# Kernel optimization log

Hardware: AMD Instinct MI355X
Metric: run time of the kernel (lower is better)

Reference implementation:

```python
import jax, jax.numpy as jnp
import numpy as np

B = 2048      # batch
C = 200       # n_country
F = 32        # n_feat_country == n_input
H = 256       # n_hidden


def setup_inputs() -> dict:
    key = jax.random.key(0)
    ks = jax.random.split(key, 9)
    x = jax.random.normal(ks[0], (B, C * F), dtype=jnp.float32)
    transition = jax.random.uniform(ks[1], (C, C), dtype=jnp.float32) / C
    W1 = jax.random.normal(ks[2], (F, H), dtype=jnp.float32) * (1.0 / np.sqrt(F))
    b1 = jax.random.normal(ks[3], (H,), dtype=jnp.float32) * 0.01
    W2 = jax.random.normal(ks[4], (H, H), dtype=jnp.float32) * (1.0 / np.sqrt(H))
    b2 = jax.random.normal(ks[5], (H,), dtype=jnp.float32) * 0.01
    W3 = jax.random.normal(ks[6], (H, 1), dtype=jnp.float32) * (1.0 / np.sqrt(H))
    b3 = jax.random.normal(ks[7], (1,), dtype=jnp.float32) * 0.01
    return {"x": x, "transition": transition, "W1": W1, "b1": b1,
            "W2": W2, "b2": b2, "W3": W3, "b3": b3}


def reference(x, transition, W1, b1, W2, b2, W3, b3):
    Bsz, N = x.shape
    Cn = transition.shape[0]
    Ff = N // Cn
    xc = x.reshape(Bsz, Cn, Ff)            # per-country feature blocks
    S = xc[..., 0]                          # [B, C] susceptible (feature 0)
    I = xc[..., 1]                          # [B, C] infected   (feature 1)
    # transition-weighted neighbor aggregation (the python loop == one GEMM)
    sinflow = S @ transition                # [B, C]
    iinflow = I @ transition                # [B, C]
    outflow = 1.0 - jnp.diag(transition)    # [C]
    # shared tiny MLP applied per country (vectorized over C)
    h = jax.nn.relu(jnp.einsum('bcf,fh->bch', xc, W1) + b1)
    h = jax.nn.relu(jnp.einsum('bch,hk->bck', h, W2) + b2)
    lamb = (jnp.einsum('bch,ho->bco', h, W3) + b3)[..., 0]  # [B, C]
    dS = -lamb * S + sinflow - outflow * S
    dI = lamb * S + iinflow - outflow * I
    # interleave: pred[:, 2i] = S_i + dS_i, pred[:, 2i+1] = I_i + dI_i
    pred = jnp.stack([S + dS, I + dI], axis=-1).reshape(Bsz, 2 * Cn)
    return pred
```

## Files before the change

kernel.cpp:

```cpp
#include <hip/hip_runtime.h>
#include <stdint.h>

#define M_ROWS 409600
#define B_CNT  2048
#define C_CNT  200
#define N_TILES (M_ROWS / 64)
#define GRID_MLP 512

typedef __attribute__((ext_vector_type(8))) short bf16x8;
typedef __attribute__((ext_vector_type(4))) float f32x4;

__device__ __forceinline__ ushort f2bf(float f) {
    uint32_t u = __float_as_uint(f);
    u += 0x7fffu + ((u >> 16) & 1u);
    return (ushort)(u >> 16);
}

__device__ __forceinline__ f32x4 mfma16(bf16x8 a, bf16x8 b, f32x4 c) {
    return __builtin_amdgcn_mfma_f32_16x16x32_bf16(a, b, c, 0, 0, 0);
}

__device__ __forceinline__ bf16x8 pack8(float4 a, float4 b) {
    bf16x8 r;
    r[0] = (short)f2bf(a.x); r[1] = (short)f2bf(a.y);
    r[2] = (short)f2bf(a.z); r[3] = (short)f2bf(a.w);
    r[4] = (short)f2bf(b.x); r[5] = (short)f2bf(b.y);
    r[6] = (short)f2bf(b.z); r[7] = (short)f2bf(b.w);
    return r;
}

__global__ __launch_bounds__(256) void prep_kernel(
    const float* __restrict__ x, const float* __restrict__ T,
    const float* __restrict__ W1, const float* __restrict__ W2,
    ushort* __restrict__ xb16, float* __restrict__ Sc, float* __restrict__ Ic,
    float* __restrict__ sinW, float* __restrict__ iinW,
    ushort* __restrict__ W1t, ushort* __restrict__ W2t, int do_xb) {
    int blk = blockIdx.x, t = threadIdx.x;
    if (blk < B_CNT) {
        __shared__ float Sr[C_CNT], Ir[C_CNT];
        const float4* xr = (const float4*)(x + (size_t)blk * 6400);
        ushort4* xw = (ushort4*)(xb16 + (size_t)blk * 6400);
#pragma unroll
        for (int i = 0; i < 7; ++i) {
            int i4 = i * 256 + t;
            if (i4 < 1600) {
                float4 v = xr[i4];
                if (do_xb) {
                    ushort4 u;
                    u.x = f2bf(v.x); u.y = f2bf(v.y);
                    u.z = f2bf(v.z); u.w = f2bf(v.w);
                    xw[i4] = u;
                }
                if ((i4 & 7) == 0) {
                    int c = i4 >> 3;
                    Sr[c] = v.x; Ir[c] = v.y;
                    Sc[blk * C_CNT + c] = v.x;
                    Ic[blk * C_CNT + c] = v.y;
                }
            }
        }
        __syncthreads();
        if (t < C_CNT) {
            float as = 0.f, ai = 0.f;
            for (int cp = 0; cp < C_CNT; ++cp) {
                float tv = T[cp * C_CNT + t];
                as = fmaf(Sr[cp], tv, as);
                ai = fmaf(Ir[cp], tv, ai);
            }
            sinW[blk * C_CNT + t] = as;
            iinW[blk * C_CNT + t] = ai;
        }
    } else if (blk < B_CNT + 256) {
        int n = blk - B_CNT;
        W2t[n * 256 + t] = f2bf(W2[t * 256 + n]);
    } else {
        int idx = (blk - B_CNT - 256) * 256 + t;
        int n = idx >> 5, k = idx & 31;
        W1t[idx] = f2bf(W1[k * 256 + n]);
    }
}

template <bool XB>
__global__ __launch_bounds__(256, 2) void mlp_kernel(
    const float* __restrict__ x,
    const ushort* __restrict__ xb16,
    const float* __restrict__ T,
    const float* __restrict__ b1,
    const float* __restrict__ b2,
    const float* __restrict__ W3,
    const float* __restrict__ b3,
    const ushort* __restrict__ W1t,
    const ushort* __restrict__ W2t,
    const float* __restrict__ Sc, const float* __restrict__ Ic,
    const float* __restrict__ sinW, const float* __restrict__ iinW,
    float* __restrict__ out) {
    constexpr int RS = 264;
    __shared__ ushort h1s[64 * RS];
    __shared__ float b1f[256], b2f[256], w3f[256];
    __shared__ float lamb_part[4][64];

    const int tid  = threadIdx.x;
    const int w    = tid >> 6;
    const int lane = tid & 63;
    const int L    = lane & 15;
    const int q    = lane >> 4;

    b1f[tid] = b1[tid];
    b2f[tid] = b2[tid];
    w3f[tid] = W3[tid];
    const float b3v = b3[0];

    bf16x8 a2r[4][8];
#pragma unroll
    for (int i2 = 0; i2 < 4; ++i2)
#pragma unroll
        for (int kc = 0; kc < 8; ++kc)
            a2r[i2][kc] =
                *(const bf16x8*)(W2t + (64 * w + i2 * 16 + L) * 256 + kc * 32 + q * 8);

    bf16x8 aw[4];
#pragma unroll
    for (int i = 0; i < 4; ++i)
        aw[i] = *(const bf16x8*)(W1t + (64 * w + i * 16 + L) * 32 + q * 8);

    for (int tile = blockIdx.x; tile < N_TILES; tile += GRID_MLP) {
        const int m0 = tile * 64;

        bf16x8 bx[4];
#pragma unroll
        for (int i = 0; i < 4; ++i) {
            if (XB) {
                bx[i] = *(const bf16x8*)(xb16 + (size_t)(m0 + i * 16 + L) * 32 + q * 8);
            } else {
                const float4* xr =
                    (const float4*)(x + (size_t)(m0 + i * 16 + L) * 32 + q * 8);
                bx[i] = pack8(xr[0], xr[1]);
            }
        }
        f32x4 acc1[4][4];
#pragma unroll
        for (int i1 = 0; i1 < 4; ++i1)
#pragma unroll
            for (int im = 0; im < 4; ++im)
                acc1[i1][im] = mfma16(aw[i1], bx[im], (f32x4){0.f, 0.f, 0.f, 0.f});

        __syncthreads();

#pragma unroll
        for (int i1 = 0; i1 < 4; ++i1) {
            int n1b = 64 * w + i1 * 16 + q * 4;
#pragma unroll
            for (int im = 0; im < 4; ++im) {
                int m = im * 16 + L;
                float v0 = fmaxf(acc1[i1][im][0] + b1f[n1b + 0], 0.f);
                float v1 = fmaxf(acc1[i1][im][1] + b1f[n1b + 1], 0.f);
                float v2 = fmaxf(acc1[i1][im][2] + b1f[n1b + 2], 0.f);
                float v3 = fmaxf(acc1[i1][im][3] + b1f[n1b + 3], 0.f);
                uint2 pk;
                pk.x = (uint32_t)f2bf(v0) | ((uint32_t)f2bf(v1) << 16);
                pk.y = (uint32_t)f2bf(v2) | ((uint32_t)f2bf(v3) << 16);
                *reinterpret_cast<uint2*>(&h1s[m * RS + n1b]) = pk;
            }
        }
        __syncthreads();

        f32x4 acc2[4][4];
#pragma unroll
        for (int i2 = 0; i2 < 4; ++i2)
#pragma unroll
            for (int im = 0; im < 4; ++im) acc2[i2][im] = (f32x4){0.f, 0.f, 0.f, 0.f};

#pragma unroll
        for (int kc = 0; kc < 8; ++kc) {
            bf16x8 bh[4];
#pragma unroll
            for (int im = 0; im < 4; ++im) {
                int m = im * 16 + L;
                bh[im] = *(const bf16x8*)(&h1s[m * RS + kc * 32 + q * 8]);
            }
#pragma unroll
            for (int i2 = 0; i2 < 4; ++i2)
#pragma unroll
                for (int im = 0; im < 4; ++im)
                    acc2[i2][im] = mfma16(a2r[i2][kc], bh[im], acc2[i2][im]);
        }

        float part[4] = {0.f, 0.f, 0.f, 0.f};
#pragma unroll
        for (int i2 = 0; i2 < 4; ++i2) {
            int n2b = 64 * w + i2 * 16 + q * 4;
#pragma unroll
            for (int im = 0; im < 4; ++im)
#pragma unroll
                for (int r = 0; r < 4; ++r) {
                    float h2 = fmaxf(acc2[i2][im][r] + b2f[n2b + r], 0.f);
                    part[im] = fmaf(h2, w3f[n2b + r], part[im]);
                }
        }
#pragma unroll
        for (int im = 0; im < 4; ++im) {
            float p = part[im];
            p += __shfl_xor(p, 16);
            p += __shfl_xor(p, 32);
            if (q == 0) lamb_part[w][im * 16 + L] = p;
        }
        __syncthreads();

        if (tid < 64) {
            int gm = m0 + tid;
            float lam = lamb_part[0][tid] + lamb_part[1][tid] +
                        lamb_part[2][tid] + lamb_part[3][tid] + b3v;
            float S = Sc[gm], I = Ic[gm];
            int c = gm % C_CNT;
            float of = 1.0f - T[c * C_CNT + c];
            float sv = sinW[gm], iv = iinW[gm];
            float dS = -lam * S + sv - of * S;
            float dI =  lam * S + iv - of * I;
            float2 o; o.x = S + dS; o.y = I + dI;
            ((float2*)out)[gm] = o;
        }
    }
}

extern "C" void kernel_launch(void* const* d_in, const int* in_sizes, int n_in,
                              void* d_out, int out_size, void* d_ws, size_t ws_size,
                              hipStream_t stream) {
    const float* x  = (const float*)d_in[0];
    const float* T  = (const float*)d_in[1];
    const float* W1 = (const float*)d_in[2];
    const float* b1 = (const float*)d_in[3];
    const float* W2 = (const float*)d_in[4];
    const float* b2 = (const float*)d_in[5];
    const float* W3 = (const float*)d_in[6];
    const float* b3 = (const float*)d_in[7];

    const size_t xb_bytes = (size_t)M_ROWS * 32 * 2;
    const size_t f32_arr  = (size_t)M_ROWS * 4;
    const size_t small    = 4 * f32_arr + 8192 * 2 + 65536 * 2;
    const int    do_xb    = (ws_size >= xb_bytes + small) ? 1 : 0;

    char* ws = (char*)d_ws;
    ushort* xb16 = (ushort*)ws;
    char* base = ws + (do_xb ? xb_bytes : 0);
    float*  Sc   = (float*)(base);
    float*  Ic   = (float*)(base + f32_arr);
    float*  sinW = (float*)(base + 2 * f32_arr);
    float*  iinW = (float*)(base + 3 * f32_arr);
    ushort* W1t  = (ushort*)(base + 4 * f32_arr);
    ushort* W2t  = (ushort*)(base + 4 * f32_arr + 8192 * 2);

    hipLaunchKernelGGL(prep_kernel, dim3(B_CNT + 256 + 32), dim3(256), 0, stream,
                       x, T, W1, W2, xb16, Sc, Ic, sinW, iinW, W1t, W2t, do_xb);
    if (do_xb) {
        hipLaunchKernelGGL((mlp_kernel<true>), dim3(GRID_MLP), dim3(256), 0, stream,
                           x, xb16, T, b1, b2, W3, b3, W1t, W2t, Sc, Ic, sinW, iinW,
                           (float*)d_out);
    } else {
        hipLaunchKernelGGL((mlp_kernel<false>), dim3(GRID_MLP), dim3(256), 0, stream,
                           x, xb16, T, b1, b2, W3, b3, W1t, W2t, Sc, Ic, sinW, iinW,
                           (float*)d_out);
    }
}
```

Baseline: 185.1 us.

## Prefetch next tile's x, defer epilogue a tile, and use packed bf16 conversion

The persistent MLP loop now loads the next tile's x fragment right after the first MFMA layer, so global load latency overlaps compute. The lambda reduction is double-buffered in shared memory, and the final epilogue for each tile runs during the next iteration, which removes one __syncthreads per tile. Smaller changes replace the manual bf16 rounding with the v_cvt_pk_bf16_f32 instruction and read biases and W3 as float4 vectors. The cost is higher register pressure from the prefetched fragments and the carried epilogue state, plus a redundant reload of the current tile on the last iteration.

```diff
diff --git a/kernel.cpp b/kernel.cpp
--- a/kernel.cpp
+++ b/kernel.cpp
@@ -14,6 +14,12 @@
     uint32_t u = __float_as_uint(f);
     u += 0x7fffu + ((u >> 16) & 1u);
     return (ushort)(u >> 16);
+}
+
+__device__ __forceinline__ uint32_t cvtpk_bf16(float lo, float hi) {
+    uint32_t r;
+    asm("v_cvt_pk_bf16_f32 %0, %1, %2" : "=v"(r) : "v"(lo), "v"(hi));
+    return r;
 }
 
 __device__ __forceinline__ f32x4 mfma16(bf16x8 a, bf16x8 b, f32x4 c) {
@@ -97,7 +103,7 @@
     constexpr int RS = 264;
     __shared__ ushort h1s[64 * RS];
     __shared__ float b1f[256], b2f[256], w3f[256];
-    __shared__ float lamb_part[4][64];
+    __shared__ float lamb2[2][4][64];
 
     const int tid  = threadIdx.x;
     const int w    = tid >> 6;
@@ -123,20 +129,24 @@
     for (int i = 0; i < 4; ++i)
         aw[i] = *(const bf16x8*)(W1t + (64 * w + i * 16 + L) * 32 + q * 8);
 
-    for (int tile = blockIdx.x; tile < N_TILES; tile += GRID_MLP) {
-        const int m0 = tile * 64;
-
-        bf16x8 bx[4];
-#pragma unroll
-        for (int i = 0; i < 4; ++i) {
-            if (XB) {
-                bx[i] = *(const bf16x8*)(xb16 + (size_t)(m0 + i * 16 + L) * 32 + q * 8);
-            } else {
-                const float4* xr =
-                    (const float4*)(x + (size_t)(m0 + i * 16 + L) * 32 + q * 8);
-                bx[i] = pack8(xr[0], xr[1]);
-            }
-        }
+    int tile = blockIdx.x;
+    bf16x8 bx[4];
+#pragma unroll
+    for (int i = 0; i < 4; ++i) {
+        if (XB) {
+            bx[i] = *(const bf16x8*)(xb16 + (size_t)(tile * 64 + i * 16 + L) * 32 + q * 8);
+        } else {
+            const float4* xr =
+                (const float4*)(x + (size_t)(tile * 64 + i * 16 + L) * 32 + q * 8);
+            bx[i] = pack8(xr[0], xr[1]);
+        }
+    }
+
+    float eS = 0.f, eI = 0.f, esv = 0.f, eiv = 0.f, eof = 0.f;
+    int ptile = -1;
+    int p = 0;
+
+    for (; tile < N_TILES; tile += GRID_MLP) {
         f32x4 acc1[4][4];
 #pragma unroll
         for (int i1 = 0; i1 < 4; ++i1)
@@ -144,24 +154,52 @@
             for (int im = 0; im < 4; ++im)
                 acc1[i1][im] = mfma16(aw[i1], bx[im], (f32x4){0.f, 0.f, 0.f, 0.f});
 
+        {
+            int tn = tile + GRID_MLP;
+            if (tn >= N_TILES) tn = tile;
+            const size_t mn0 = (size_t)tn * 64;
+#pragma unroll
+            for (int i = 0; i < 4; ++i) {
+                if (XB) {
+                    bx[i] = *(const bf16x8*)(xb16 + (mn0 + i * 16 + L) * 32 + q * 8);
+                } else {
+                    const float4* xr =
+                        (const float4*)(x + (mn0 + i * 16 + L) * 32 + q * 8);
+                    bx[i] = pack8(xr[0], xr[1]);
+                }
+            }
+        }
+
         __syncthreads();
 
 #pragma unroll
         for (int i1 = 0; i1 < 4; ++i1) {
             int n1b = 64 * w + i1 * 16 + q * 4;
+            const float4 bv = *reinterpret_cast<const float4*>(&b1f[n1b]);
 #pragma unroll
             for (int im = 0; im < 4; ++im) {
                 int m = im * 16 + L;
-                float v0 = fmaxf(acc1[i1][im][0] + b1f[n1b + 0], 0.f);
-                float v1 = fmaxf(acc1[i1][im][1] + b1f[n1b + 1], 0.f);
-                float v2 = fmaxf(acc1[i1][im][2] + b1f[n1b + 2], 0.f);
-                float v3 = fmaxf(acc1[i1][im][3] + b1f[n1b + 3], 0.f);
+                float v0 = fmaxf(acc1[i1][im][0] + bv.x, 0.f);
+                float v1 = fmaxf(acc1[i1][im][1] + bv.y, 0.f);
+                float v2 = fmaxf(acc1[i1][im][2] + bv.z, 0.f);
+                float v3 = fmaxf(acc1[i1][im][3] + bv.w, 0.f);
                 uint2 pk;
-                pk.x = (uint32_t)f2bf(v0) | ((uint32_t)f2bf(v1) << 16);
-                pk.y = (uint32_t)f2bf(v2) | ((uint32_t)f2bf(v3) << 16);
+                pk.x = cvtpk_bf16(v0, v1);
+                pk.y = cvtpk_bf16(v2, v3);
                 *reinterpret_cast<uint2*>(&h1s[m * RS + n1b]) = pk;
             }
         }
+
+        if (ptile >= 0 && tid < 64) {
+            int gm = ptile * 64 + tid;
+            float lam = lamb2[p ^ 1][0][tid] + lamb2[p ^ 1][1][tid] +
+                        lamb2[p ^ 1][2][tid] + lamb2[p ^ 1][3][tid] + b3v;
+            float dS = -lam * eS + esv - eof * eS;
+            float dI =  lam * eS + eiv - eof * eI;
+            float2 o; o.x = eS + dS; o.y = eI + dI;
+            ((float2*)out)[gm] = o;
+        }
+
         __syncthreads();
 
         f32x4 acc2[4][4];
@@ -185,40 +223,53 @@
                     acc2[i2][im] = mfma16(a2r[i2][kc], bh[im], acc2[i2][im]);
         }
 
+        if (tid < 64) {
+            int gm = tile * 64 + tid;
+            eS  = Sc[gm];  eI  = Ic[gm];
+            esv = sinW[gm]; eiv = iinW[gm];
+            int c = gm % C_CNT;
+            eof = 1.0f - T[c * C_CNT + c];
+        }
+
         float part[4] = {0.f, 0.f, 0.f, 0.f};
 #pragma unroll
         for (int i2 = 0; i2 < 4; ++i2) {
             int n2b = 64 * w + i2 * 16 + q * 4;
-#pragma unroll
-            for (int im = 0; im < 4; ++im)
-#pragma unroll
-                for (int r = 0; r < 4; ++r) {
-                    float h2 = fmaxf(acc2[i2][im][r] + b2f[n2b + r], 0.f);
-                    part[im] = fmaf(h2, w3f[n2b + r], part[im]);
-                }
+            const float4 b2v = *reinterpret_cast<const float4*>(&b2f[n2b]);
+            const float4 w3v = *reinterpret_cast<const float4*>(&w3f[n2b]);
+#pragma unroll
+            for (int im = 0; im < 4; ++im) {
+                float h0 = fmaxf(acc2[i2][im][0] + b2v.x, 0.f);
+                float h1 = fmaxf(acc2[i2][im][1] + b2v.y, 0.f);
+                float h2 = fmaxf(acc2[i2][im][2] + b2v.z, 0.f);
+                float h3 = fmaxf(acc2[i2][im][3] + b2v.w, 0.f);
+                part[im] = fmaf(h0, w3v.x, part[im]);
+                part[im] = fmaf(h1, w3v.y, part[im]);
+                part[im] = fmaf(h2, w3v.z, part[im]);
+                part[im] = fmaf(h3, w3v.w, part[im]);
+            }
         }
 #pragma unroll
         for (int im = 0; im < 4; ++im) {
-            float p = part[im];
-            p += __shfl_xor(p, 16);
-            p += __shfl_xor(p, 32);
-            if (q == 0) lamb_part[w][im * 16 + L] = p;
-        }
-        __syncthreads();
-
-        if (tid < 64) {
-            int gm = m0 + tid;
-            float lam = lamb_part[0][tid] + lamb_part[1][tid] +
-                        lamb_part[2][tid] + lamb_part[3][tid] + b3v;
-            float S = Sc[gm], I = Ic[gm];
-            int c = gm % C_CNT;
-            float of = 1.0f - T[c * C_CNT + c];
-            float sv = sinW[gm], iv = iinW[gm];
-            float dS = -lam * S + sv - of * S;
-            float dI =  lam * S + iv - of * I;
-            float2 o; o.x = S + dS; o.y = I + dI;
-            ((float2*)out)[gm] = o;
-        }
+            float pp = part[im];
+            pp += __shfl_xor(pp, 16);
+            pp += __shfl_xor(pp, 32);
+            if (q == 0) lamb2[p][w][im * 16 + L] = pp;
+        }
+
+        ptile = tile;
+        p ^= 1;
+    }
+
+    __syncthreads();
+    if (ptile >= 0 && tid < 64) {
+        int gm = ptile * 64 + tid;
+        float lam = lamb2[p ^ 1][0][tid] + lamb2[p ^ 1][1][tid] +
+                    lamb2[p ^ 1][2][tid] + lamb2[p ^ 1][3][tid] + b3v;
+        float dS = -lam * eS + esv - eof * eS;
+        float dI =  lam * eS + eiv - eof * eI;
+        float2 o; o.x = eS + dS; o.y = eI + dI;
+        ((float2*)out)[gm] = o;
     }
 }
 
```

Result: slower. 202.0 us (+9.1%).
